# Kernel optimization log

Measured on AMD Instinct MI355X. Metric: run time of the kernel, lower is better.

Reference implementation:

```python
import jax, jax.numpy as jnp
import numpy as np

DIM = 512
MOVE_EMBED_DIM = 64
NUM_BUCKETS = 64
EMBED = 768
B = 8192
STEPS = 10


def setup_inputs() -> dict:
    key = jax.random.key(0)
    ks = jax.random.split(key, 16)
    def g(i, shape, scale=0.02):
        return jax.random.normal(ks[i], shape, jnp.float32) * scale
    return {
        "boards": jax.random.normal(ks[0], (STEPS, B, EMBED), jnp.float32),
        "flags": jax.random.randint(ks[1], (STEPS - 2, B), 0, 2).astype(bool),
        "themes": jax.random.randint(ks[2], (B,), 0, 10),
        "moves": jax.random.randint(ks[3], (B,), 0, NUM_BUCKETS),
        "start": jax.random.uniform(ks[4], (DIM,), jnp.float32),
        "red_w": g(5, (DIM, EMBED)), "red_b": jnp.zeros((DIM,), jnp.float32),
        "ca_w": g(6, (DIM, DIM)), "ca_b": jnp.zeros((DIM,), jnp.float32),
        "cb_w": g(7, (DIM, DIM)), "cb_b": jnp.zeros((DIM,), jnp.float32),
        "move_emb": g(8, (NUM_BUCKETS, MOVE_EMBED_DIM), 1.0),
        "fc1_w": g(9, (DIM, DIM + MOVE_EMBED_DIM)), "fc1_b": jnp.zeros((DIM,), jnp.float32),
        "fc2_w": g(10, (DIM, DIM)), "fc2_b": jnp.zeros((DIM,), jnp.float32),
        "fc3_w": g(11, (1024, DIM)), "fc3_b": jnp.zeros((1024,), jnp.float32),
        "fc4_w": g(12, (1024, 1024)), "fc4_b": jnp.zeros((1024,), jnp.float32),
        "fc5_w": g(13, (512, 1024)), "fc5_b": jnp.zeros((512,), jnp.float32),
        "out_w": g(14, (1, 512)), "out_b": jnp.zeros((1,), jnp.float32),
    }


def reference(boards, flags, themes, moves, start, red_w, red_b, ca_w, ca_b,
              cb_w, cb_b, move_emb, fc1_w, fc1_b, fc2_w, fc2_b, fc3_w, fc3_b,
              fc4_w, fc4_b, fc5_w, fc5_b, out_w, out_b):
    bsz = boards.shape[1]
    # boards[0:2] are never masked; boards[2:10] are zeroed where flags are False
    full_flags = jnp.concatenate([jnp.ones((2, bsz), bool), flags], axis=0)  # [10,B]
    emb = jnp.where(full_flags[:, :, None], boards, 0.0)                     # [10,B,E]
    # shared dim reducer + relu applied to all 10 positions at once
    e = jax.nn.relu(jnp.einsum('sbe,de->sbd', emb, red_w) + red_b)           # [10,B,DIM]
    # precompute combiner_b contribution for every step (batched GEMM)
    eb = jnp.einsum('sbd,kd->sbk', e, cb_w) + cb_b                           # [10,B,DIM]
    # combiner_a(start)+combiner_b(e0) == combiner_a(h0)+... with h0 = start broadcast
    h0 = jnp.broadcast_to(start, (bsz, DIM))
    def step(h, eb_t):
        return jnp.tanh(h @ ca_w.T + ca_b + eb_t), None
    h, _ = jax.lax.scan(step, h0, eb)                                        # [B,DIM]
    # dropout layers are identity in eval mode
    m = move_emb[moves]                                                      # [B,MOVE_EMBED_DIM]
    x = jax.nn.relu(jnp.concatenate([h, m], axis=-1) @ fc1_w.T + fc1_b)
    x = jax.nn.relu(x @ fc2_w.T + fc2_b)
    x = jax.nn.relu(x @ fc3_w.T + fc3_b)
    x = jax.nn.relu(x @ fc4_w.T + fc4_b)
    x = jax.nn.relu(x @ fc5_w.T + fc5_b)
    return x @ out_w.T + out_b                                               # [B,1]
```

## Files before the change

### kernel.cpp

```cpp
#include <hip/hip_runtime.h>
#include <math.h>

#define BATCH  8192
#define EMBED  768
#define DIMD   512
#define MEDIM  64
#define NSTEP  10

typedef __bf16 bf16x8 __attribute__((ext_vector_type(8)));
typedef float  f32x4  __attribute__((ext_vector_type(4)));

__device__ __forceinline__ void load16_lds(const __bf16* g, __bf16* l)
{
    auto* gp = (__attribute__((address_space(1))) char*)(uintptr_t)(const void*)g;
    auto* lp = (__attribute__((address_space(3))) char*)(unsigned int)(uintptr_t)(void*)l;
    __builtin_amdgcn_global_load_lds(gp, lp, 16, 0, 0);
}

#define BN 128
#define BK 32

template<int ACT, bool ADDEB, bool GATHER, int BMT>
__global__ __launch_bounds__(256)
void gemm_bf16(const __bf16* __restrict__ A, const __bf16* __restrict__ Bt,
               const float* __restrict__ bias, const __bf16* __restrict__ add,
               const __bf16* __restrict__ me, const int* __restrict__ moves,
               __bf16* __restrict__ C, int M, int N, int K)
{
    constexpr int NG = (BMT + BN) / 16;
    constexpr int AG = BMT / 16;
    constexpr int MR = BMT / 32;

    __shared__ __bf16 lds[(BMT + BN) * BK];

    const int nwg  = gridDim.x * gridDim.y;
    const int orig = blockIdx.y * gridDim.x + blockIdx.x;
    const int cpx  = nwg >> 3;
    const int swz  = (orig & 7) * cpx + (orig >> 3);
    const int bx   = swz % gridDim.x;
    const int by   = swz / gridDim.x;

    const int tid  = threadIdx.x;
    const int wave = tid >> 6;
    const int lane = tid & 63;
    const int row0 = by * BMT;
    const int col0 = bx * BN;

    const int wr = (wave >> 1) * (BMT / 2);
    const int wc = (wave & 1) * 64;
    const int fr = lane & 15;
    const int fk = (lane >> 4) * 8;

    const int srow = lane >> 2;
    const int skk  = (lane & 3) * 8;

    f32x4 acc[MR][4] = {};

    for (int k0 = 0; k0 < K; k0 += BK) {
#pragma unroll
        for (int ci = 0; ci < NG / 4; ++ci) {
            const int c = ci * 4 + wave;
            const int r = c * 16 + srow;
            const __bf16* g;
            if (c < AG) {
                if (GATHER) {
                    const int grow = row0 + r;
                    g = (k0 < DIMD)
                        ? (A  + (size_t)grow * DIMD + k0 + skk)
                        : (me + (size_t)moves[grow] * MEDIM + (k0 - DIMD) + skk);
                } else {
                    g = A + (size_t)(row0 + r) * K + k0 + skk;
                }
            } else {
                g = Bt + (size_t)(col0 + (r - BMT)) * K + k0 + skk;
            }
            load16_lds(g, &lds[c * 512]);
        }
        __syncthreads();

        const __bf16* As = lds;
        const __bf16* Bs = lds + BMT * BK;
        bf16x8 af[MR], bfr[4];
#pragma unroll
        for (int m = 0; m < MR; ++m)
            af[m] = *(const bf16x8*)&As[(wr + m * 16 + fr) * BK + fk];
#pragma unroll
        for (int n = 0; n < 4; ++n)
            bfr[n] = *(const bf16x8*)&Bs[(wc + n * 16 + fr) * BK + fk];
#pragma unroll
        for (int m = 0; m < MR; ++m)
#pragma unroll
            for (int n = 0; n < 4; ++n)
                acc[m][n] = __builtin_amdgcn_mfma_f32_16x16x32_bf16(
                                af[m], bfr[n], acc[m][n], 0, 0, 0);
        __syncthreads();
    }

#pragma unroll
    for (int m = 0; m < MR; ++m) {
#pragma unroll
        for (int n = 0; n < 4; ++n) {
            const int cc = col0 + wc + n * 16 + fr;
            const float bb = bias[cc];
#pragma unroll
            for (int j = 0; j < 4; ++j) {
                const int rr = row0 + wr + m * 16 + (lane >> 4) * 4 + j;
                float v = acc[m][n][j] + bb;
                if (ADDEB) v += (float)add[(size_t)rr * N + cc];
                if (ACT == 1) v = fmaxf(v, 0.0f);
                if (ACT == 2) {
                    const float p = __expf(2.0f * v);
                    v = 1.0f - 2.0f / (p + 1.0f);
                }
                C[(size_t)rr * N + cc] = (__bf16)v;
            }
        }
    }
}

__global__ __launch_bounds__(256)
void cvt_boards_all(const float* __restrict__ src, const int* __restrict__ flags,
                    __bf16* __restrict__ dst)
{
    const int idx  = blockIdx.x * 256 + threadIdx.x;
    const int grow = idx / 96;
    const int s    = grow >> 13;
    const int b    = grow & 8191;
    float m = 1.0f;
    if (s >= 2) m = flags[(size_t)(s - 2) * BATCH + b] ? 1.0f : 0.0f;
    const float4 v0 = ((const float4*)src)[(size_t)idx * 2];
    const float4 v1 = ((const float4*)src)[(size_t)idx * 2 + 1];
    bf16x8 o;
    o[0] = (__bf16)(v0.x * m); o[1] = (__bf16)(v0.y * m);
    o[2] = (__bf16)(v0.z * m); o[3] = (__bf16)(v0.w * m);
    o[4] = (__bf16)(v1.x * m); o[5] = (__bf16)(v1.y * m);
    o[6] = (__bf16)(v1.z * m); o[7] = (__bf16)(v1.w * m);
    *(bf16x8*)(dst + (size_t)idx * 8) = o;
}

enum : int { W_RED = 0, W_CA = 393216, W_CB = 655360, W_FC1 = 917504,
             W_FC2 = 1212416, W_FC3 = 1474560, W_FC4 = 1998848,
             W_FC5 = 3047424, W_ME = 3571712, W_TOTAL = 3575808 };

__global__ __launch_bounds__(256)
void cvt_weights(const float* __restrict__ w0, const float* __restrict__ w1,
                 const float* __restrict__ w2, const float* __restrict__ w3,
                 const float* __restrict__ w4, const float* __restrict__ w5,
                 const float* __restrict__ w6, const float* __restrict__ w7,
                 const float* __restrict__ w8, __bf16* __restrict__ dst)
{
    const int idx = blockIdx.x * 256 + threadIdx.x;
    if (idx >= W_TOTAL / 8) return;
    const int e = idx * 8;
    const float* src; int off;
    if      (e < W_CA)  { src = w0; off = W_RED; }
    else if (e < W_CB)  { src = w1; off = W_CA; }
    else if (e < W_FC1) { src = w2; off = W_CB; }
    else if (e < W_FC2) { src = w3; off = W_FC1; }
    else if (e < W_FC3) { src = w4; off = W_FC2; }
    else if (e < W_FC4) { src = w5; off = W_FC3; }
    else if (e < W_FC5) { src = w6; off = W_FC4; }
    else if (e < W_ME)  { src = w7; off = W_FC5; }
    else                { src = w8; off = W_ME; }
    const float4 v0 = ((const float4*)(src + (e - off)))[0];
    const float4 v1 = ((const float4*)(src + (e - off)))[1];
    bf16x8 o;
    o[0] = (__bf16)v0.x; o[1] = (__bf16)v0.y; o[2] = (__bf16)v0.z; o[3] = (__bf16)v0.w;
    o[4] = (__bf16)v1.x; o[5] = (__bf16)v1.y; o[6] = (__bf16)v1.z; o[7] = (__bf16)v1.w;
    *(bf16x8*)(dst + (size_t)e) = o;
}

__global__ __launch_bounds__(256)
void gemv_start(const float* __restrict__ caw, const float* __restrict__ cab,
                const float* __restrict__ start, float* __restrict__ tmp)
{
    __shared__ float s[DIMD];
    for (int i = threadIdx.x; i < DIMD; i += 256) s[i] = start[i];
    __syncthreads();
    const int n = blockIdx.x * 256 + threadIdx.x;
    const float4* w = (const float4*)(caw + (size_t)n * DIMD);
    float acc = 0.0f;
#pragma unroll 8
    for (int k = 0; k < DIMD / 4; ++k) {
        const float4 wv = w[k];
        acc += wv.x * s[k * 4] + wv.y * s[k * 4 + 1] +
               wv.z * s[k * 4 + 2] + wv.w * s[k * 4 + 3];
    }
    tmp[n] = acc + cab[n];
}

__global__ __launch_bounds__(256)
void h1_init(const float* __restrict__ tmp, const __bf16* __restrict__ eb0,
             __bf16* __restrict__ h)
{
    const int idx = blockIdx.x * 256 + threadIdx.x;
    const int c8 = idx & 63;
    const bf16x8 e = ((const bf16x8*)eb0)[idx];
    bf16x8 o;
#pragma unroll
    for (int j = 0; j < 8; ++j) {
        const float v = tmp[c8 * 8 + j] + (float)e[j];
        const float p = __expf(2.0f * v);
        o[j] = (__bf16)(1.0f - 2.0f / (p + 1.0f));
    }
    ((bf16x8*)h)[idx] = o;
}

__global__ __launch_bounds__(256)
void out_head(const __bf16* __restrict__ x, const float* __restrict__ out_w,
              const float* __restrict__ out_b, float* __restrict__ out)
{
    const int wid  = threadIdx.x >> 6;
    const int lane = threadIdx.x & 63;
    const int row  = blockIdx.x * 4 + wid;
    const bf16x8 xv = *(const bf16x8*)(x + (size_t)row * DIMD + lane * 8);
    const float4 w0 = ((const float4*)out_w)[lane * 2];
    const float4 w1 = ((const float4*)out_w)[lane * 2 + 1];
    float s = (float)xv[0] * w0.x + (float)xv[1] * w0.y + (float)xv[2] * w0.z +
              (float)xv[3] * w0.w + (float)xv[4] * w1.x + (float)xv[5] * w1.y +
              (float)xv[6] * w1.z + (float)xv[7] * w1.w;
#pragma unroll
    for (int off = 32; off; off >>= 1) s += __shfl_down(s, off, 64);
    if (lane == 0) out[row] = s + out_b[0];
}

extern "C" void kernel_launch(void* const* d_in, const int* in_sizes, int n_in,
                              void* d_out, int out_size, void* d_ws, size_t ws_size,
                              hipStream_t stream)
{
    const float* boards  = (const float*)d_in[0];
    const int*   flags   = (const int*)  d_in[1];
    const int*   moves   = (const int*)  d_in[3];
    const float* start   = (const float*)d_in[4];
    const float* red_w   = (const float*)d_in[5];
    const float* red_b   = (const float*)d_in[6];
    const float* ca_w    = (const float*)d_in[7];
    const float* ca_b    = (const float*)d_in[8];
    const float* cb_w    = (const float*)d_in[9];
    const float* cb_b    = (const float*)d_in[10];
    const float* move_emb= (const float*)d_in[11];
    const float* fc1_w   = (const float*)d_in[12];
    const float* fc1_b   = (const float*)d_in[13];
    const float* fc2_w   = (const float*)d_in[14];
    const float* fc2_b   = (const float*)d_in[15];
    const float* fc3_w   = (const float*)d_in[16];
    const float* fc3_b   = (const float*)d_in[17];
    const float* fc4_w   = (const float*)d_in[18];
    const float* fc4_b   = (const float*)d_in[19];
    const float* fc5_w   = (const float*)d_in[20];
    const float* fc5_b   = (const float*)d_in[21];
    const float* out_w   = (const float*)d_in[22];
    const float* out_b   = (const float*)d_in[23];

    __bf16* wsb = (__bf16*)d_ws;
    __bf16* wpool  = wsb;
    __bf16* b_all  = wsb + 3575808;
    __bf16* e_all  = wsb + 66490368;
    __bf16* eb_all = wsb + 108433408;
    __bf16* hA     = wsb + 150376448;
    __bf16* hB     = wsb + 154570752;
    float*  tmpv   = (float*)(wsb + 158765056);
    __bf16* x1     = wsb + 159789056;
    __bf16* x2     = wsb + 163983360;
    __bf16* x3     = wsb + 168177664;
    __bf16* x4     = wsb + 176566272;
    __bf16* x5     = wsb + 184954880;

    const dim3 blk(256);

    cvt_weights<<<1746, blk, 0, stream>>>(red_w, ca_w, cb_w, fc1_w, fc2_w,
                                          fc3_w, fc4_w, fc5_w, move_emb, wpool);
    cvt_boards_all<<<30720, blk, 0, stream>>>(boards, flags, b_all);
    gemv_start<<<2, blk, 0, stream>>>(ca_w, ca_b, start, tmpv);

    gemm_bf16<1, false, false, 128><<<dim3(4, 640), blk, 0, stream>>>(
        b_all, wpool + W_RED, red_b, nullptr, nullptr, nullptr, e_all,
        NSTEP * BATCH, DIMD, EMBED);
    gemm_bf16<0, false, false, 128><<<dim3(4, 640), blk, 0, stream>>>(
        e_all, wpool + W_CB, cb_b, nullptr, nullptr, nullptr, eb_all,
        NSTEP * BATCH, DIMD, DIMD);

    h1_init<<<2048, blk, 0, stream>>>(tmpv, eb_all, hA);

    __bf16* hcur = hA;
    __bf16* hnxt = hB;
    for (int s = 1; s < NSTEP; ++s) {
        const __bf16* ebs = eb_all + (size_t)s * BATCH * DIMD;
        gemm_bf16<2, true, false, 64><<<dim3(4, 128), blk, 0, stream>>>(
            hcur, wpool + W_CA, ca_b, ebs, nullptr, nullptr, hnxt,
            BATCH, DIMD, DIMD);
        __bf16* t = hcur; hcur = hnxt; hnxt = t;
    }

    gemm_bf16<1, false, true, 128><<<dim3(4, 64), blk, 0, stream>>>(
        hcur, wpool + W_FC1, fc1_b, nullptr, wpool + W_ME, moves, x1,
        BATCH, DIMD, DIMD + MEDIM);
    gemm_bf16<1, false, false, 128><<<dim3(4, 64), blk, 0, stream>>>(
        x1, wpool + W_FC2, fc2_b, nullptr, nullptr, nullptr, x2, BATCH, DIMD, DIMD);
    gemm_bf16<1, false, false, 128><<<dim3(8, 64), blk, 0, stream>>>(
        x2, wpool + W_FC3, fc3_b, nullptr, nullptr, nullptr, x3, BATCH, 1024, DIMD);
    gemm_bf16<1, false, false, 128><<<dim3(8, 64), blk, 0, stream>>>(
        x3, wpool + W_FC4, fc4_b, nullptr, nullptr, nullptr, x4, BATCH, 1024, 1024);
    gemm_bf16<1, false, false, 128><<<dim3(4, 64), blk, 0, stream>>>(
        x4, wpool + W_FC5, fc5_b, nullptr, nullptr, nullptr, x5, BATCH, DIMD, 1024);

    out_head<<<BATCH / 4, blk, 0, stream>>>(x5, out_w, out_b, (float*)d_out);
}
```

Measured before the change: 524.5 us.

## Fuse board masking and bf16 conversion into reducer GEMM A-tile loads

Drops the separate pass that masked and converted the fp32 boards to bf16. A new reducer GEMM loads fp32 board tiles straight into LDS with an XOR swizzle, applies the per-row flag mask and converts to bf16 in registers before the MFMA. This removes a large intermediate write and re-read, at the cost of doubling the A-operand bytes per tile and adding conversion work inside the GEMM loop.

```diff
diff --git a/kernel.cpp b/kernel.cpp
--- a/kernel.cpp
+++ b/kernel.cpp
@@ -10,10 +10,10 @@
 typedef __bf16 bf16x8 __attribute__((ext_vector_type(8)));
 typedef float  f32x4  __attribute__((ext_vector_type(4)));
 
-__device__ __forceinline__ void load16_lds(const __bf16* g, __bf16* l)
-{
-    auto* gp = (__attribute__((address_space(1))) char*)(uintptr_t)(const void*)g;
-    auto* lp = (__attribute__((address_space(3))) char*)(unsigned int)(uintptr_t)(void*)l;
+__device__ __forceinline__ void load16_lds(const void* g, void* l)
+{
+    auto* gp = (__attribute__((address_space(1))) char*)(uintptr_t)g;
+    auto* lp = (__attribute__((address_space(3))) char*)(unsigned int)(uintptr_t)l;
     __builtin_amdgcn_global_load_lds(gp, lp, 16, 0, 0);
 }
 
@@ -119,23 +119,101 @@
 }
 
 __global__ __launch_bounds__(256)
-void cvt_boards_all(const float* __restrict__ src, const int* __restrict__ flags,
-                    __bf16* __restrict__ dst)
-{
-    const int idx  = blockIdx.x * 256 + threadIdx.x;
-    const int grow = idx / 96;
-    const int s    = grow >> 13;
-    const int b    = grow & 8191;
-    float m = 1.0f;
-    if (s >= 2) m = flags[(size_t)(s - 2) * BATCH + b] ? 1.0f : 0.0f;
-    const float4 v0 = ((const float4*)src)[(size_t)idx * 2];
-    const float4 v1 = ((const float4*)src)[(size_t)idx * 2 + 1];
-    bf16x8 o;
-    o[0] = (__bf16)(v0.x * m); o[1] = (__bf16)(v0.y * m);
-    o[2] = (__bf16)(v0.z * m); o[3] = (__bf16)(v0.w * m);
-    o[4] = (__bf16)(v1.x * m); o[5] = (__bf16)(v1.y * m);
-    o[6] = (__bf16)(v1.z * m); o[7] = (__bf16)(v1.w * m);
-    *(bf16x8*)(dst + (size_t)idx * 8) = o;
+void gemm_red_f32A(const float* __restrict__ A, const __bf16* __restrict__ Bt,
+                   const float* __restrict__ bias, const int* __restrict__ flags,
+                   __bf16* __restrict__ C, int M, int N, int K)
+{
+    __shared__ float  Af[128 * 32];
+    __shared__ __bf16 Bs[128 * 32];
+
+    const int nwg  = gridDim.x * gridDim.y;
+    const int orig = blockIdx.y * gridDim.x + blockIdx.x;
+    const int cpx  = nwg >> 3;
+    const int swz  = (orig & 7) * cpx + (orig >> 3);
+    const int bx   = swz % gridDim.x;
+    const int by   = swz / gridDim.x;
+
+    const int tid  = threadIdx.x;
+    const int wave = tid >> 6;
+    const int lane = tid & 63;
+    const int row0 = by * 128;
+    const int col0 = bx * BN;
+
+    const int wr = (wave >> 1) * 64;
+    const int wc = (wave & 1) * 64;
+    const int fr = lane & 15;
+    const int fk = (lane >> 4) * 8;
+
+    const int asrow = lane >> 3;
+    const int akc   = (lane & 7) ^ asrow;
+    const int bsrow = lane >> 2;
+    const int bskk  = (lane & 3) * 8;
+
+    float am[4];
+#pragma unroll
+    for (int m = 0; m < 4; ++m) {
+        const int r = row0 + wr + m * 16 + fr;
+        const int s = r >> 13, b = r & 8191;
+        am[m] = (s < 2) ? 1.0f : (flags[(size_t)(s - 2) * BATCH + b] ? 1.0f : 0.0f);
+    }
+
+    f32x4 acc[4][4] = {};
+
+    for (int k0 = 0; k0 < K; k0 += BK) {
+#pragma unroll
+        for (int ci = 0; ci < 6; ++ci) {
+            const int c = ci * 4 + wave;
+            if (c < 16) {
+                const float* g = A + (size_t)(row0 + c * 8 + asrow) * K + k0 + akc * 4;
+                load16_lds(g, (char*)Af + c * 1024);
+            } else {
+                const int cb = c - 16;
+                const __bf16* g = Bt + (size_t)(col0 + cb * 16 + bsrow) * K + k0 + bskk;
+                load16_lds(g, (char*)Bs + cb * 1024);
+            }
+        }
+        __syncthreads();
+
+        bf16x8 af[4], bfr[4];
+#pragma unroll
+        for (int m = 0; m < 4; ++m) {
+            const int r = wr + m * 16 + fr;
+            const int kc0 = fk >> 2;
+            const f32x4 v0 = *(const f32x4*)&Af[r * 32 + ((kc0    ) ^ (r & 7)) * 4];
+            const f32x4 v1 = *(const f32x4*)&Af[r * 32 + ((kc0 + 1) ^ (r & 7)) * 4];
+            const float mk = am[m];
+#pragma unroll
+            for (int j = 0; j < 4; ++j) {
+                af[m][j]     = (__bf16)(v0[j] * mk);
+                af[m][j + 4] = (__bf16)(v1[j] * mk);
+            }
+        }
+#pragma unroll
+        for (int n = 0; n < 4; ++n)
+            bfr[n] = *(const bf16x8*)&Bs[(wc + n * 16 + fr) * BK + fk];
+#pragma unroll
+        for (int m = 0; m < 4; ++m)
+#pragma unroll
+            for (int n = 0; n < 4; ++n)
+                acc[m][n] = __builtin_amdgcn_mfma_f32_16x16x32_bf16(
+                                af[m], bfr[n], acc[m][n], 0, 0, 0);
+        __syncthreads();
+    }
+
+#pragma unroll
+    for (int m = 0; m < 4; ++m) {
+#pragma unroll
+        for (int n = 0; n < 4; ++n) {
+            const int cc = col0 + wc + n * 16 + fr;
+            const float bb = bias[cc];
+#pragma unroll
+            for (int j = 0; j < 4; ++j) {
+                const int rr = row0 + wr + m * 16 + (lane >> 4) * 4 + j;
+                float v = fmaxf(acc[m][n][j] + bb, 0.0f);
+                C[(size_t)rr * N + cc] = (__bf16)v;
+            }
+        }
+    }
 }
 
 enum : int { W_RED = 0, W_CA = 393216, W_CB = 655360, W_FC1 = 917504,
@@ -254,28 +332,25 @@
 
     __bf16* wsb = (__bf16*)d_ws;
     __bf16* wpool  = wsb;
-    __bf16* b_all  = wsb + 3575808;
-    __bf16* e_all  = wsb + 66490368;
-    __bf16* eb_all = wsb + 108433408;
-    __bf16* hA     = wsb + 150376448;
-    __bf16* hB     = wsb + 154570752;
-    float*  tmpv   = (float*)(wsb + 158765056);
-    __bf16* x1     = wsb + 159789056;
-    __bf16* x2     = wsb + 163983360;
-    __bf16* x3     = wsb + 168177664;
-    __bf16* x4     = wsb + 176566272;
-    __bf16* x5     = wsb + 184954880;
+    __bf16* e_all  = wsb + 3575808;
+    __bf16* eb_all = wsb + 45518848;
+    __bf16* hA     = wsb + 87461888;
+    __bf16* hB     = wsb + 91656192;
+    float*  tmpv   = (float*)(wsb + 95850496);
+    __bf16* x1     = wsb + 96874496;
+    __bf16* x2     = wsb + 101068800;
+    __bf16* x3     = wsb + 105263104;
+    __bf16* x4     = wsb + 113651712;
+    __bf16* x5     = wsb + 122040320;
 
     const dim3 blk(256);
 
     cvt_weights<<<1746, blk, 0, stream>>>(red_w, ca_w, cb_w, fc1_w, fc2_w,
                                           fc3_w, fc4_w, fc5_w, move_emb, wpool);
-    cvt_boards_all<<<30720, blk, 0, stream>>>(boards, flags, b_all);
     gemv_start<<<2, blk, 0, stream>>>(ca_w, ca_b, start, tmpv);
 
-    gemm_bf16<1, false, false, 128><<<dim3(4, 640), blk, 0, stream>>>(
-        b_all, wpool + W_RED, red_b, nullptr, nullptr, nullptr, e_all,
-        NSTEP * BATCH, DIMD, EMBED);
+    gemm_red_f32A<<<dim3(4, 640), blk, 0, stream>>>(
+        boards, wpool + W_RED, red_b, flags, e_all, NSTEP * BATCH, DIMD, EMBED);
     gemm_bf16<0, false, false, 128><<<dim3(4, 640), blk, 0, stream>>>(
         e_all, wpool + W_CB, cb_b, nullptr, nullptr, nullptr, eb_all,
         NSTEP * BATCH, DIMD, DIMD);
```

Measured after the change: 494.0 us. 5.8% less time.

## Double-buffer LDS tiles in bf16 GEMM and XOR-swizzle k-chunks

Applied to the files above, without the earlier changes.

The GEMM kernel now keeps two LDS buffers and issues the global-to-LDS loads for the next K tile before computing on the current one, so memory latency overlaps with MFMA work and one barrier per iteration goes away. It also XOR-swizzles the 8-element k-chunk position per row when staging and when reading fragments, to cut LDS bank conflicts. The cost is doubled LDS use per block, which may lower occupancy. It also relies on the single remaining barrier to order the async direct-to-LDS loads correctly.

```diff
diff --git a/kernel.cpp b/kernel.cpp
--- a/kernel.cpp
+++ b/kernel.cpp
@@ -10,10 +10,10 @@
 typedef __bf16 bf16x8 __attribute__((ext_vector_type(8)));
 typedef float  f32x4  __attribute__((ext_vector_type(4)));
 
-__device__ __forceinline__ void load16_lds(const __bf16* g, __bf16* l)
-{
-    auto* gp = (__attribute__((address_space(1))) char*)(uintptr_t)(const void*)g;
-    auto* lp = (__attribute__((address_space(3))) char*)(unsigned int)(uintptr_t)(void*)l;
+__device__ __forceinline__ void load16_lds(const void* g, void* l)
+{
+    auto* gp = (__attribute__((address_space(1))) char*)(uintptr_t)g;
+    auto* lp = (__attribute__((address_space(3))) char*)(unsigned int)(uintptr_t)l;
     __builtin_amdgcn_global_load_lds(gp, lp, 16, 0, 0);
 }
 
@@ -31,7 +31,7 @@
     constexpr int AG = BMT / 16;
     constexpr int MR = BMT / 32;
 
-    __shared__ __bf16 lds[(BMT + BN) * BK];
+    __shared__ __bf16 lds[2][(BMT + BN) * BK];
 
     const int nwg  = gridDim.x * gridDim.y;
     const int orig = blockIdx.y * gridDim.x + blockIdx.x;
@@ -49,14 +49,12 @@
     const int wr = (wave >> 1) * (BMT / 2);
     const int wc = (wave & 1) * 64;
     const int fr = lane & 15;
-    const int fk = (lane >> 4) * 8;
+    const int q  = lane >> 4;
 
     const int srow = lane >> 2;
-    const int skk  = (lane & 3) * 8;
-
-    f32x4 acc[MR][4] = {};
-
-    for (int k0 = 0; k0 < K; k0 += BK) {
+    const int skk  = (((lane & 3) ^ ((lane >> 3) & 3)) * 8);
+
+    auto stage = [&](int buf, int k0) {
 #pragma unroll
         for (int ci = 0; ci < NG / 4; ++ci) {
             const int c = ci * 4 + wave;
@@ -74,19 +72,33 @@
             } else {
                 g = Bt + (size_t)(col0 + (r - BMT)) * K + k0 + skk;
             }
-            load16_lds(g, &lds[c * 512]);
+            load16_lds(g, &lds[buf][c * 512]);
         }
-        __syncthreads();
-
-        const __bf16* As = lds;
-        const __bf16* Bs = lds + BMT * BK;
+    };
+
+    auto frag = [&](const __bf16* base, int r) -> bf16x8 {
+        return *(const bf16x8*)&base[r * 32 + ((q ^ ((r >> 1) & 3)) << 3)];
+    };
+
+    f32x4 acc[MR][4] = {};
+
+    stage(0, 0);
+    __syncthreads();
+
+    const int NT = K / BK;
+    int cur = 0;
+    for (int t = 0; t < NT; ++t) {
+        if (t + 1 < NT) stage(cur ^ 1, (t + 1) * BK);
+
+        const __bf16* As = lds[cur];
+        const __bf16* Bs = lds[cur] + BMT * BK;
         bf16x8 af[MR], bfr[4];
 #pragma unroll
         for (int m = 0; m < MR; ++m)
-            af[m] = *(const bf16x8*)&As[(wr + m * 16 + fr) * BK + fk];
+            af[m] = frag(As, wr + m * 16 + fr);
 #pragma unroll
         for (int n = 0; n < 4; ++n)
-            bfr[n] = *(const bf16x8*)&Bs[(wc + n * 16 + fr) * BK + fk];
+            bfr[n] = frag(Bs, wc + n * 16 + fr);
 #pragma unroll
         for (int m = 0; m < MR; ++m)
 #pragma unroll
@@ -94,6 +106,7 @@
                 acc[m][n] = __builtin_amdgcn_mfma_f32_16x16x32_bf16(
                                 af[m], bfr[n], acc[m][n], 0, 0, 0);
         __syncthreads();
+        cur ^= 1;
     }
 
 #pragma unroll
```

Measured after the change: 470.5 us. -10.3%, faster.
